# Performance work log

Measured on AMD Instinct MI355X. Metric: run time of the kernel, lower is better.

## Reference

```python
import jax, jax.numpy as jnp
import numpy as np

TAU = 2.0      # LIF time constant
VTH = 1.0      # spike threshold
ALPHA = 4.0    # sigmoid surrogate slope (spikingjelly default)
EPS = 1e-5     # BN eps

@jax.custom_vjp
def spike_fn(x):
    return (x >= 0.0).astype(x.dtype)

def _spike_fwd(x):
    return spike_fn(x), x

def _spike_bwd(x, g):
    s = jax.nn.sigmoid(ALPHA * x)
    return (g * ALPHA * s * (1.0 - s),)

spike_fn.defvjp(_spike_fwd, _spike_bwd)

def conv2d(x, w, stride=1):
    return jax.lax.conv_general_dilated(
        x, w, (stride, stride), 'SAME',
        dimension_numbers=('NCHW', 'OIHW', 'NCHW'))

def bn(x, g, b, m, v):
    # eval-mode BatchNorm2d over channel axis 1
    scale = g / jnp.sqrt(v + EPS)
    return (x - m[:, None, None]) * scale[:, None, None] + b[:, None, None]

def lif_step(v, x):
    # charge, fire, hard reset to 0 (detach_reset)
    v = v + (x - v) / TAU
    s = spike_fn(v - VTH)
    v = (1.0 - jax.lax.stop_gradient(s)) * v
    return v, s

def lif_multistep(x_seq):
    v0 = jnp.zeros_like(x_seq[0])
    _, s = jax.lax.scan(lif_step, v0, x_seq)
    return s

def setup_inputs():
    key = jax.random.key(0)
    ks = jax.random.split(key, 8)
    T, B, C, H, W = 4, 4, 2, 128, 128
    E = 256
    x = jax.random.normal(ks[0], (T, B, C, H, W), jnp.float32)
    w_proj = jax.random.normal(ks[1], (E // 2, C, 3, 3), jnp.float32) * 0.2
    w_temp = jax.random.normal(ks[2], (C, E // 2, 3, 3), jnp.float32) * 0.05
    w1 = jax.random.normal(ks[3], (E, E // 2, 3, 3), jnp.float32) * 0.03
    w_res = jax.random.normal(ks[4], (E, E // 2, 1, 1), jnp.float32) * 0.09
    def bn_params(k, c):
        kk = jax.random.split(k, 2)
        return (jnp.abs(jax.random.normal(kk[0], (c,), jnp.float32)) + 0.5,
                jax.random.normal(kk[1], (c,), jnp.float32) * 0.1,
                jnp.zeros((c,), jnp.float32), jnp.ones((c,), jnp.float32))
    g0, b0, m0, v0 = bn_params(ks[5], E // 2)
    gt, bt, mt, vt = bn_params(ks[6], C)
    g1, b1, m1, v1 = bn_params(ks[7], E)
    gr, br, mr, vr = bn_params(jax.random.fold_in(key, 99), E)
    return dict(x=x, w_proj=w_proj, g0=g0, b0=b0, m0=m0, v0=v0,
                w_temp=w_temp, gt=gt, bt=bt, mt=mt, vt=vt,
                w1=w1, g1=g1, b1=b1, m1=m1, v1=v1,
                w_res=w_res, gr=gr, br=br, mr=mr, vr=vr)

def reference(x, w_proj, g0, b0, m0, v0, w_temp, gt, bt, mt, vt,
              w1, g1, b1, m1, v1, w_res, gr, br, mr, vr):
    T, B, C, H, W = x.shape
    half = w_proj.shape[0]
    # stf_1 recurrent coding: x_in[t] = x[t] + x_out[t-1]; LIF states persist
    def step(carry, x_t):
        x_out, vp, vtm = carry
        x_in = x_t + x_out
        h = bn(conv2d(x_in, w_proj), g0, b0, m0, v0)          # [B,half,H,W]
        vp, s1 = lif_step(vp, h)                              # proj_lif
        y = bn(conv2d(s1, w_temp), gt, bt, mt, vt)            # [B,C,H,W]
        vtm, s2 = lif_step(vtm, y)                            # proj_temporal_lif
        return (s2, vp, vtm), s1
    init = (jnp.zeros((B, C, H, W), x.dtype),
            jnp.zeros((B, half, H, W), x.dtype),
            jnp.zeros((B, C, H, W), x.dtype))
    _, spikes = jax.lax.scan(step, init, x)                   # [T,B,half,H,W]
    xf = spikes.reshape(T * B, half, H, W)
    xa = bn(conv2d(xf, w1), g1, b1, m1, v1).reshape(T, B, -1, H, W)
    xa = lif_multistep(xa)                                    # proj1_lif
    xr = bn(conv2d(xf, w_res), gr, br, mr, vr).reshape(T, B, -1, H, W)
    xr = lif_multistep(xr)                                    # proj_res_lif
    return xa + xr
```

## Files before the change

### kernel.cpp

```cpp
#include <hip/hip_runtime.h>
#include <math.h>

#define HW 16384

typedef __attribute__((ext_vector_type(8))) _Float16 half8;
typedef __attribute__((ext_vector_type(4))) float f32x4;

__global__ __launch_bounds__(256)
void k_reorder2(const float* __restrict__ w1, const float* __restrict__ wres,
                const float* __restrict__ g1, const float* __restrict__ b1,
                const float* __restrict__ m1, const float* __restrict__ v1,
                const float* __restrict__ gr, const float* __restrict__ br,
                const float* __restrict__ mr, const float* __restrict__ vr,
                const float* __restrict__ g0, const float* __restrict__ v0,
                const float* __restrict__ gt, const float* __restrict__ vt,
                short* __restrict__ whi, short* __restrict__ wmid,
                short* __restrict__ rhi, short* __restrict__ rmid,
                float* __restrict__ bias1, float* __restrict__ biasr,
                float* __restrict__ psc, float* __restrict__ tsc) {
    int i = blockIdx.x * 256 + threadIdx.x;
    if (i < 294912) {
        int n = i / 1152, rem = i % 1152;
        int ic = rem / 9, tap = rem % 9;
        float sc = g1[n] / sqrtf(v1[n] + 1e-5f);
        float wv = (w1[i] * sc) * 4096.0f;
        _Float16 h = (_Float16)wv;
        float r1 = wv - (float)h;
        _Float16 m = (_Float16)r1;
        int kb = ic >> 5, q = (ic >> 3) & 3, j = ic & 7;
        size_t f = ((((size_t)(kb * 9 + tap)) * 4 + q) * 256 + n) * 8 + j;
        whi[f]  = __builtin_bit_cast(short, h);
        wmid[f] = __builtin_bit_cast(short, m);
    }
    if (i < 32768) {
        int n = i >> 7, ic = i & 127;
        float sc = gr[n] / sqrtf(vr[n] + 1e-5f);
        float wv = (wres[i] * sc) * 4096.0f;
        _Float16 h = (_Float16)wv;
        float r1 = wv - (float)h;
        _Float16 m = (_Float16)r1;
        int kb = ic >> 5, q = (ic >> 3) & 3, j = ic & 7;
        size_t f = (((size_t)kb * 4 + q) * 256 + n) * 8 + j;
        rhi[f]  = __builtin_bit_cast(short, h);
        rmid[f] = __builtin_bit_cast(short, m);
    }
    if (i < 256) {
        float sc1 = g1[i] / sqrtf(v1[i] + 1e-5f);
        bias1[i] = (b1[i] - m1[i] * sc1) * 4096.0f;
        float scr_ = gr[i] / sqrtf(vr[i] + 1e-5f);
        biasr[i] = (br[i] - mr[i] * scr_) * 4096.0f;
    }
    if (i < 128) psc[i] = g0[i] / sqrtf(v0[i] + 1e-5f);
    if (i < 2)   tsc[i] = gt[i] / sqrtf(vt[i] + 1e-5f);
}

__global__ __launch_bounds__(256)
void k_proj(const float* __restrict__ xt, const float* __restrict__ xout,
            const float* __restrict__ wp,
            const float* __restrict__ psc, const float* __restrict__ bb,
            const float* __restrict__ mm,
            float* __restrict__ vp, unsigned char* __restrict__ s1t,
            int first, int last) {
    __shared__ float xin[2 * 10 * 36];
    const int tid = threadIdx.x;
    const int b   = blockIdx.z >> 2;
    const int ocq = blockIdx.z & 3;
    const int gy0 = blockIdx.y * 8, gx0 = blockIdx.x * 32;

    for (int i = tid; i < 680; i += 256) {
        int ch = i / 340, rem = i % 340;
        int r = rem / 34, c = rem % 34;
        int gy = gy0 - 1 + r, gx = gx0 - 1 + c;
        float val = 0.f;
        if (gy >= 0 && gy < 128 && gx >= 0 && gx < 128) {
            int idx = ((b * 2 + ch) << 14) + (gy << 7) + gx;
            val = xt[idx];
            if (!first) val += xout[idx];
        }
        xin[(ch * 10 + r) * 36 + c] = val;
    }
    __syncthreads();

    const int prow = tid >> 5, pcol = tid & 31;
    float xw[2][3][3];
#pragma unroll
    for (int ch = 0; ch < 2; ++ch)
#pragma unroll
        for (int ky = 0; ky < 3; ++ky)
#pragma unroll
            for (int kx = 0; kx < 3; ++kx)
                xw[ch][ky][kx] = xin[(ch * 10 + prow + ky) * 36 + pcol + kx];

    const int pix = ((gy0 + prow) << 7) + gx0 + pcol;
    const int oc_beg = ocq * 32;
    unsigned int pk = 0u;
#pragma unroll
    for (int oo = 0; oo < 32; ++oo) {
        const int oc = oc_beg + oo;
        float acc = 0.f;
#pragma unroll
        for (int ch = 0; ch < 2; ++ch)
#pragma unroll
            for (int ky = 0; ky < 3; ++ky)
#pragma unroll
                for (int kx = 0; kx < 3; ++kx)
                    acc = fmaf(wp[((oc * 2 + ch) * 3 + ky) * 3 + kx], xw[ch][ky][kx], acc);
        float sc = psc[oc];
        float h  = (acc - mm[oc]) * sc + bb[oc];
        int idx = ((b * 128 + oc) << 14) + pix;
        float v = first ? 0.f : vp[idx];
        v = v + (h - v) * 0.5f;
        bool s = (v >= 1.0f);
        if (!last) vp[idx] = s ? 0.f : v;
        pk |= (s ? 1u : 0u) << oo;
    }
    *(unsigned int*)(s1t + ((((size_t)b << 14) + pix) << 4) + ocq * 4) = pk;
}

__global__ __launch_bounds__(256)
void k_temp(const unsigned char* __restrict__ s1t, const float* __restrict__ wt,
            const float* __restrict__ tsc, const float* __restrict__ bb,
            const float* __restrict__ mm,
            float* __restrict__ vtm, float* __restrict__ xout,
            int first, int lastv) {
    __shared__ unsigned char sl[49152];
    __shared__ float wls[2304];
    __shared__ float red[256];
    const int tid = threadIdx.x;
    const int b   = blockIdx.y;
    const int y0  = blockIdx.x;

    for (int i = tid; i < 2304; i += 256) wls[i] = wt[i];

    for (int i = tid; i < 384; i += 256) {
        int r = i >> 7, px = i & 127;
        int gy = y0 - 1 + r;
        uint4 d = make_uint4(0u, 0u, 0u, 0u);
        if (gy >= 0 && gy < 128)
            d = *(const uint4*)(s1t + ((((size_t)b << 14) + (gy << 7) + px) << 4));
        unsigned int bs[4] = {d.x, d.y, d.z, d.w};
#pragma unroll
        for (int icb = 0; icb < 16; ++icb) {
            unsigned int v8 = (bs[icb >> 2] >> ((icb & 3) * 8)) & 0xFFu;
            unsigned int lo = (v8 & 1u) | ((v8 & 2u) << 7) | ((v8 & 4u) << 14) | ((v8 & 8u) << 21);
            unsigned int hi = ((v8 >> 4) & 1u) | ((v8 & 32u) << 3) | ((v8 & 64u) << 10) | ((v8 & 128u) << 17);
            *(uint2*)&sl[(((icb * 3) + r) * 128 + (px ^ (icb & 7))) * 8] = make_uint2(lo, hi);
        }
    }
    __syncthreads();

    const int x = tid & 127, hf = tid >> 7;
    float a0 = 0.f, a1 = 0.f;
#pragma unroll 1
    for (int ii = 0; ii < 8; ++ii) {
        const int icb = hf * 8 + ii;
        int sw = icb & 7;
        const float* w0 = &wls[icb * 72];
        const float* w1_ = &wls[1152 + icb * 72];
#pragma unroll
        for (int dy = 0; dy < 3; ++dy) {
#pragma unroll
            for (int dx = 0; dx < 3; ++dx) {
                int xx = x - 1 + dx;
                if (xx < 0 || xx > 127) continue;
                uint2 d = *(const uint2*)&sl[((icb * 3 + dy) * 128 + (xx ^ sw)) * 8];
                int tap = dy * 3 + dx;
#pragma unroll
                for (int j = 0; j < 4; ++j) {
                    float f0 = (float)((d.x >> (8 * j)) & 0xFFu);
                    float f1 = (float)((d.y >> (8 * j)) & 0xFFu);
                    a0 = fmaf(w0[j * 9 + tap],        f0, a0);
                    a0 = fmaf(w0[(4 + j) * 9 + tap],  f1, a0);
                    a1 = fmaf(w1_[j * 9 + tap],       f0, a1);
                    a1 = fmaf(w1_[(4 + j) * 9 + tap], f1, a1);
                }
            }
        }
    }
    if (hf) { red[x] = a0; red[128 + x] = a1; }
    __syncthreads();
    if (!hf) {
        a0 += red[x]; a1 += red[128 + x];
#pragma unroll
        for (int oc = 0; oc < 2; ++oc) {
            float acc = (oc == 0) ? a0 : a1;
            float sc = tsc[oc];
            float yv = (acc - mm[oc]) * sc + bb[oc];
            int idx = ((b * 2 + oc) << 14) + (y0 << 7) + x;
            float v = first ? 0.f : vtm[idx];
            v = v + (yv - v) * 0.5f;
            bool s = (v >= 1.0f);
            if (!lastv) vtm[idx] = s ? 0.f : v;
            xout[idx] = s ? 1.0f : 0.f;
        }
    }
}

__global__ __launch_bounds__(256, 3)
void k_fused(const unsigned char* __restrict__ s1c,
             const short* __restrict__ whi, const short* __restrict__ wmid,
             const short* __restrict__ rhi, const short* __restrict__ rmid,
             const float* __restrict__ bias1, const float* __restrict__ biasr,
             float* __restrict__ out) {
    __shared__ __align__(16) unsigned char bl[8704];
    __shared__ __align__(16) unsigned char xp[34816];

    const int tid = threadIdx.x;
    const int oc0 = blockIdx.x * 64;
    const int yb = blockIdx.y;
    const int b = yb >> 8, ry = (yb >> 2) & 63, cx = yb & 3;
    const int gy0 = ry * 2, gx0 = cx * 32;

    const int w   = tid >> 6, l = tid & 63;
    const int q   = l >> 4,  ln = l & 15;
    const int woc = w >> 1,  wpx = w & 1;

    const size_t wofs = ((size_t)q * 256 + oc0 + woc * 32 + ln) * 8;

    int pb[2], po[2], eb[2];
#pragma unroll
    for (int nt = 0; nt < 2; ++nt) {
        int px = wpx * 32 + nt * 16 + ln;
        int prow = px >> 5, pcol = px & 31;
        pb[nt] = prow * 34 + pcol;
        po[nt] = ((gy0 + prow) << 7) + gx0 + pcol;
        eb[nt] = pb[nt] * 64 + q * 16;
    }

    for (int cc = tid; cc < 544; cc += 256) {
        int t = cc / 136, p = cc - t * 136;
        int r = p / 34, c = p - r * 34;
        int gy = gy0 - 1 + r, gx = gx0 - 1 + c;
        uint4 d = make_uint4(0u, 0u, 0u, 0u);
        if (gy >= 0 && gy < 128 && gx >= 0 && gx < 128)
            d = *(const uint4*)(s1c + (size_t)t * 1048576 +
                                ((((size_t)b << 14) + (gy << 7) + gx) << 4));
        *(uint4*)(bl + cc * 16) = d;
    }
    __syncthreads();

    const float ds_ = 0.000244140625f;

    unsigned int srb[4];
    {
        f32x4 brr[2];
#pragma unroll
        for (int mt = 0; mt < 2; ++mt)
#pragma unroll
            for (int rg = 0; rg < 4; ++rg)
                brr[mt][rg] = biasr[oc0 + woc * 32 + mt * 16 + q * 4 + rg];

        float vres[2][2][4];
#pragma unroll
        for (int nt = 0; nt < 2; ++nt)
#pragma unroll
            for (int mt = 0; mt < 2; ++mt)
#pragma unroll
                for (int rg = 0; rg < 4; ++rg) vres[nt][mt][rg] = 0.f;

#pragma unroll
        for (int t = 0; t < 4; ++t) {
            const unsigned char* blt = bl + t * 2176;
            f32x4 accr[2][2];
#pragma unroll
            for (int nt = 0; nt < 2; ++nt)
#pragma unroll
                for (int mt = 0; mt < 2; ++mt) accr[nt][mt] = brr[mt];

#pragma unroll
            for (int kb = 0; kb < 4; ++kb) {
                half8 B4[2];
#pragma unroll
                for (int nt = 0; nt < 2; ++nt) {
                    unsigned int v8 = blt[(pb[nt] + 35) * 16 + kb * 4 + q];
                    uint4 pk;
                    pk.x = ((v8 & 1u)          | ((v8 & 2u)   << 15)) * 0x3C00u;
                    pk.y = (((v8 >> 2) & 1u)   | ((v8 & 8u)   << 13)) * 0x3C00u;
                    pk.z = (((v8 >> 4) & 1u)   | ((v8 & 32u)  << 11)) * 0x3C00u;
                    pk.w = (((v8 >> 6) & 1u)   | ((v8 & 128u) << 9 )) * 0x3C00u;
                    B4[nt] = __builtin_bit_cast(half8, pk);
                }
                half8 RH[2], RM[2];
#pragma unroll
                for (int mt = 0; mt < 2; ++mt) {
                    RH[mt] = *(const half8*)(rhi  + wofs + (size_t)kb * 8192 + mt * 128);
                    RM[mt] = *(const half8*)(rmid + wofs + (size_t)kb * 8192 + mt * 128);
                }
#pragma unroll
                for (int nt = 0; nt < 2; ++nt)
#pragma unroll
                    for (int mt = 0; mt < 2; ++mt) {
                        accr[nt][mt] = __builtin_amdgcn_mfma_f32_16x16x32_f16(RH[mt], B4[nt], accr[nt][mt], 0, 0, 0);
                        accr[nt][mt] = __builtin_amdgcn_mfma_f32_16x16x32_f16(RM[mt], B4[nt], accr[nt][mt], 0, 0, 0);
                    }
            }

            unsigned int sb = 0u;
#pragma unroll
            for (int nt = 0; nt < 2; ++nt)
#pragma unroll
                for (int mt = 0; mt < 2; ++mt)
#pragma unroll
                    for (int rg = 0; rg < 4; ++rg) {
                        float hr = accr[nt][mt][rg] * ds_;
                        float u = vres[nt][mt][rg];
                        u = u + (hr - u) * 0.5f;
                        bool sr_ = (u >= 1.0f);
                        vres[nt][mt][rg] = sr_ ? 0.f : u;
                        sb |= (sr_ ? 1u : 0u) << (mt * 8 + rg * 2 + nt);
                    }
            srb[t] = sb;
        }
    }

    f32x4 acc[4][2][2];
#pragma unroll
    for (int mt = 0; mt < 2; ++mt)
#pragma unroll
        for (int rg = 0; rg < 4; ++rg) {
            float bv = bias1[oc0 + woc * 32 + mt * 16 + q * 4 + rg];
#pragma unroll
            for (int t = 0; t < 4; ++t)
#pragma unroll
                for (int nt = 0; nt < 2; ++nt) acc[t][nt][mt][rg] = bv;
        }

    const short* bh = whi  + wofs;
    const short* bm = wmid + wofs;
#pragma unroll 1
    for (int kb = 0; kb < 4; ++kb) {
        if (kb) __syncthreads();
        for (int cc = tid; cc < 2176; cc += 256) {
            int r = cc >> 2, c = cc & 3;
            unsigned int dw = *(const unsigned int*)(bl + r * 16 + kb * 4);
            unsigned int x0 = dw >> (c * 8);
            uint4 o;
            o.x = ((x0 & 1u)          | ((x0 & 2u)   << 15)) * 0x3C00u;
            o.y = (((x0 >> 2) & 1u)   | ((x0 & 8u)   << 13)) * 0x3C00u;
            o.z = (((x0 >> 4) & 1u)   | ((x0 & 32u)  << 11)) * 0x3C00u;
            o.w = (((x0 >> 6) & 1u)   | ((x0 & 128u) << 9 )) * 0x3C00u;
            *(uint4*)(xp + cc * 16) = o;
        }
        __syncthreads();

#pragma unroll
        for (int tap = 0; tap < 9; ++tap) {
            const int toff = ((tap / 3) * 34 + (tap % 3)) * 64;
            half8 AH[2], AM[2];
#pragma unroll
            for (int mt = 0; mt < 2; ++mt) {
                AH[mt] = *(const half8*)(bh + mt * 128);
                AM[mt] = *(const half8*)(bm + mt * 128);
            }
#pragma unroll
            for (int t = 0; t < 4; ++t) {
                half8 B4[2];
#pragma unroll
                for (int nt = 0; nt < 2; ++nt)
                    B4[nt] = *(const half8*)(xp + t * 8704 + eb[nt] + toff);
#pragma unroll
                for (int nt = 0; nt < 2; ++nt)
#pragma unroll
                    for (int mt = 0; mt < 2; ++mt) {
                        acc[t][nt][mt] = __builtin_amdgcn_mfma_f32_16x16x32_f16(AH[mt], B4[nt], acc[t][nt][mt], 0, 0, 0);
                        acc[t][nt][mt] = __builtin_amdgcn_mfma_f32_16x16x32_f16(AM[mt], B4[nt], acc[t][nt][mt], 0, 0, 0);
                    }
            }
            bh += 8192; bm += 8192;
        }
    }

    float va[2][2][4];
#pragma unroll
    for (int nt = 0; nt < 2; ++nt)
#pragma unroll
        for (int mt = 0; mt < 2; ++mt)
#pragma unroll
            for (int rg = 0; rg < 4; ++rg) va[nt][mt][rg] = 0.f;

#pragma unroll
    for (int t = 0; t < 4; ++t) {
        const size_t tb = ((size_t)((t * 4 + b) * 256 + oc0)) << 14;
#pragma unroll
        for (int mt = 0; mt < 2; ++mt)
#pragma unroll
            for (int rg = 0; rg < 4; ++rg) {
                const size_t ob = tb + ((size_t)(woc * 32 + mt * 16 + q * 4 + rg) << 14);
#pragma unroll
                for (int nt = 0; nt < 2; ++nt) {
                    float ha = acc[t][nt][mt][rg] * ds_;
                    float v = va[nt][mt][rg];
                    v = v + (ha - v) * 0.5f;
                    bool s = (v >= 1.0f);
                    va[nt][mt][rg] = s ? 0.f : v;
                    float sa = s ? 1.f : 0.f;
                    float sr = ((srb[t] >> (mt * 8 + rg * 2 + nt)) & 1u) ? 1.f : 0.f;
                    out[ob + po[nt]] = sa + sr;
                }
            }
    }
}

extern "C" void kernel_launch(void* const* d_in, const int* in_sizes, int n_in,
                              void* d_out, int out_size, void* d_ws, size_t ws_size,
                              hipStream_t stream) {
    const float* x      = (const float*)d_in[0];
    const float* w_proj = (const float*)d_in[1];
    const float* g0 = (const float*)d_in[2];
    const float* b0 = (const float*)d_in[3];
    const float* m0 = (const float*)d_in[4];
    const float* v0 = (const float*)d_in[5];
    const float* w_temp = (const float*)d_in[6];
    const float* gt = (const float*)d_in[7];
    const float* bt = (const float*)d_in[8];
    const float* mt = (const float*)d_in[9];
    const float* vt = (const float*)d_in[10];
    const float* w1 = (const float*)d_in[11];
    const float* g1 = (const float*)d_in[12];
    const float* b1 = (const float*)d_in[13];
    const float* m1 = (const float*)d_in[14];
    const float* v1 = (const float*)d_in[15];
    const float* w_res = (const float*)d_in[16];
    const float* gr = (const float*)d_in[17];
    const float* br = (const float*)d_in[18];
    const float* mr = (const float*)d_in[19];
    const float* vr = (const float*)d_in[20];

    char* ws = (char*)d_ws;
    unsigned char* s1c = (unsigned char*)ws;
    float* vp    = (float*)(ws + 4194304);
    float* vtm   = (float*)(ws + 37748736);
    float* xout  = (float*)(ws + 38273024);
    short* whi   = (short*)(ws + 38797312);
    short* wmid  = (short*)(ws + 39387136);
    short* rhi   = (short*)(ws + 39976960);
    short* rmid  = (short*)(ws + 40042496);
    float* bias1 = (float*)(ws + 40108032);
    float* biasr = (float*)(ws + 40109056);
    float* psc   = (float*)(ws + 40110080);
    float* tsc   = (float*)(ws + 40110592);

    k_reorder2<<<dim3(1152), dim3(256), 0, stream>>>(
        w1, w_res, g1, b1, m1, v1, gr, br, mr, vr, g0, v0, gt, vt,
        whi, wmid, rhi, rmid, bias1, biasr, psc, tsc);

    for (int t = 0; t < 4; ++t) {
        const float* xt = x + (size_t)t * 131072;
        unsigned char* s1t = s1c + (size_t)t * 1048576;
        k_proj<<<dim3(4, 16, 16), dim3(256), 0, stream>>>(
            xt, xout, w_proj, psc, b0, m0, vp, s1t, t == 0, t == 3);
        if (t < 3)
            k_temp<<<dim3(128, 4), dim3(256), 0, stream>>>(
                s1t, w_temp, tsc, bt, mt, vtm, xout, t == 0, t == 2);
    }

    k_fused<<<dim3(4, 1024), dim3(256), 0, stream>>>(
        s1c, whi, wmid, rhi, rmid, bias1, biasr, (float*)d_out);
}
```

Before: 618.0 us.

## Merge reorder, proj and temporal stages into one persistent kernel with grid barriers

Replaces the weight-reorder kernel and the seven per-timestep proj/temp launches with a single persistent kernel of 512 blocks. The blocks loop over tiles and separate the stages with a software grid barrier built on atomics. This removes the launch overhead and idle gaps between the small sequential kernels. In exchange it relies on all 512 blocks being co-resident (launch_bounds 256,2 with about 58KB of shared memory per block) to avoid deadlock, and it adds barrier spin cost.

Result: slower. 1.237 ms (+100.2%).

```diff
diff --git a/kernel.cpp b/kernel.cpp
--- a/kernel.cpp
+++ b/kernel.cpp
@@ -2,24 +2,55 @@
 #include <math.h>
 
 #define HW 16384
+#define NBLK 512
 
 typedef __attribute__((ext_vector_type(8))) _Float16 half8;
 typedef __attribute__((ext_vector_type(4))) float f32x4;
 
-__global__ __launch_bounds__(256)
-void k_reorder2(const float* __restrict__ w1, const float* __restrict__ wres,
-                const float* __restrict__ g1, const float* __restrict__ b1,
-                const float* __restrict__ m1, const float* __restrict__ v1,
-                const float* __restrict__ gr, const float* __restrict__ br,
-                const float* __restrict__ mr, const float* __restrict__ vr,
-                const float* __restrict__ g0, const float* __restrict__ v0,
-                const float* __restrict__ gt, const float* __restrict__ vt,
-                short* __restrict__ whi, short* __restrict__ wmid,
-                short* __restrict__ rhi, short* __restrict__ rmid,
-                float* __restrict__ bias1, float* __restrict__ biasr,
-                float* __restrict__ psc, float* __restrict__ tsc) {
-    int i = blockIdx.x * 256 + threadIdx.x;
-    if (i < 294912) {
+__device__ __forceinline__ void gsync(unsigned* bar, unsigned* lgen) {
+    __syncthreads();
+    if (threadIdx.x == 0) {
+        unsigned target = ++(*lgen);
+        __threadfence();
+        unsigned a = __hip_atomic_fetch_add(&bar[0], 1u, __ATOMIC_ACQ_REL,
+                                            __HIP_MEMORY_SCOPE_AGENT);
+        if (a == NBLK - 1) {
+            __hip_atomic_store(&bar[0], 0u, __ATOMIC_RELAXED, __HIP_MEMORY_SCOPE_AGENT);
+            __hip_atomic_fetch_add(&bar[1], 1u, __ATOMIC_RELEASE, __HIP_MEMORY_SCOPE_AGENT);
+        } else {
+            while (__hip_atomic_load(&bar[1], __ATOMIC_ACQUIRE,
+                                     __HIP_MEMORY_SCOPE_AGENT) < target)
+                __builtin_amdgcn_s_sleep(8);
+        }
+    }
+    __syncthreads();
+}
+
+__global__ __launch_bounds__(256, 2)
+void k_stage(const float* __restrict__ x, const float* __restrict__ wp,
+             const float* __restrict__ g0, const float* __restrict__ b0,
+             const float* __restrict__ m0, const float* __restrict__ v0,
+             const float* __restrict__ wt, const float* __restrict__ gt,
+             const float* __restrict__ bt, const float* __restrict__ mt,
+             const float* __restrict__ vt,
+             const float* __restrict__ w1, const float* __restrict__ g1,
+             const float* __restrict__ b1, const float* __restrict__ m1,
+             const float* __restrict__ v1,
+             const float* __restrict__ wres, const float* __restrict__ gr,
+             const float* __restrict__ br, const float* __restrict__ mr,
+             const float* __restrict__ vr,
+             unsigned char* __restrict__ s1c, float* __restrict__ vp,
+             float* __restrict__ vtm, float* xout,
+             short* __restrict__ whi, short* __restrict__ wmid,
+             short* __restrict__ rhi, short* __restrict__ rmid,
+             float* __restrict__ bias1, float* __restrict__ biasr,
+             float* __restrict__ psc, float* __restrict__ tsc,
+             unsigned* bar) {
+    __shared__ __align__(16) unsigned char smem[59392];
+    const int rb = blockIdx.x, tid = threadIdx.x;
+    unsigned lgen = 0;
+
+    for (int i = rb * 256 + tid; i < 294912; i += NBLK * 256) {
         int n = i / 1152, rem = i % 1152;
         int ic = rem / 9, tap = rem % 9;
         float sc = g1[n] / sqrtf(v1[n] + 1e-5f);
@@ -32,166 +63,169 @@
         whi[f]  = __builtin_bit_cast(short, h);
         wmid[f] = __builtin_bit_cast(short, m);
     }
-    if (i < 32768) {
-        int n = i >> 7, ic = i & 127;
-        float sc = gr[n] / sqrtf(vr[n] + 1e-5f);
-        float wv = (wres[i] * sc) * 4096.0f;
-        _Float16 h = (_Float16)wv;
-        float r1 = wv - (float)h;
-        _Float16 m = (_Float16)r1;
-        int kb = ic >> 5, q = (ic >> 3) & 3, j = ic & 7;
-        size_t f = (((size_t)kb * 4 + q) * 256 + n) * 8 + j;
-        rhi[f]  = __builtin_bit_cast(short, h);
-        rmid[f] = __builtin_bit_cast(short, m);
-    }
-    if (i < 256) {
-        float sc1 = g1[i] / sqrtf(v1[i] + 1e-5f);
-        bias1[i] = (b1[i] - m1[i] * sc1) * 4096.0f;
-        float scr_ = gr[i] / sqrtf(vr[i] + 1e-5f);
-        biasr[i] = (br[i] - mr[i] * scr_) * 4096.0f;
-    }
-    if (i < 128) psc[i] = g0[i] / sqrtf(v0[i] + 1e-5f);
-    if (i < 2)   tsc[i] = gt[i] / sqrtf(vt[i] + 1e-5f);
-}
-
-__global__ __launch_bounds__(256)
-void k_proj(const float* __restrict__ xt, const float* __restrict__ xout,
-            const float* __restrict__ wp,
-            const float* __restrict__ psc, const float* __restrict__ bb,
-            const float* __restrict__ mm,
-            float* __restrict__ vp, unsigned char* __restrict__ s1t,
-            int first, int last) {
-    __shared__ float xin[2 * 10 * 36];
-    const int tid = threadIdx.x;
-    const int b   = blockIdx.z >> 2;
-    const int ocq = blockIdx.z & 3;
-    const int gy0 = blockIdx.y * 8, gx0 = blockIdx.x * 32;
-
-    for (int i = tid; i < 680; i += 256) {
-        int ch = i / 340, rem = i % 340;
-        int r = rem / 34, c = rem % 34;
-        int gy = gy0 - 1 + r, gx = gx0 - 1 + c;
-        float val = 0.f;
-        if (gy >= 0 && gy < 128 && gx >= 0 && gx < 128) {
-            int idx = ((b * 2 + ch) << 14) + (gy << 7) + gx;
-            val = xt[idx];
-            if (!first) val += xout[idx];
-        }
-        xin[(ch * 10 + r) * 36 + c] = val;
-    }
-    __syncthreads();
-
-    const int prow = tid >> 5, pcol = tid & 31;
-    float xw[2][3][3];
-#pragma unroll
-    for (int ch = 0; ch < 2; ++ch)
-#pragma unroll
-        for (int ky = 0; ky < 3; ++ky)
-#pragma unroll
-            for (int kx = 0; kx < 3; ++kx)
-                xw[ch][ky][kx] = xin[(ch * 10 + prow + ky) * 36 + pcol + kx];
-
-    const int pix = ((gy0 + prow) << 7) + gx0 + pcol;
-    const int oc_beg = ocq * 32;
-    unsigned int pk = 0u;
-#pragma unroll
-    for (int oo = 0; oo < 32; ++oo) {
-        const int oc = oc_beg + oo;
-        float acc = 0.f;
-#pragma unroll
-        for (int ch = 0; ch < 2; ++ch)
-#pragma unroll
-            for (int ky = 0; ky < 3; ++ky)
-#pragma unroll
-                for (int kx = 0; kx < 3; ++kx)
-                    acc = fmaf(wp[((oc * 2 + ch) * 3 + ky) * 3 + kx], xw[ch][ky][kx], acc);
-        float sc = psc[oc];
-        float h  = (acc - mm[oc]) * sc + bb[oc];
-        int idx = ((b * 128 + oc) << 14) + pix;
-        float v = first ? 0.f : vp[idx];
-        v = v + (h - v) * 0.5f;
-        bool s = (v >= 1.0f);
-        if (!last) vp[idx] = s ? 0.f : v;
-        pk |= (s ? 1u : 0u) << oo;
-    }
-    *(unsigned int*)(s1t + ((((size_t)b << 14) + pix) << 4) + ocq * 4) = pk;
-}
-
-__global__ __launch_bounds__(256)
-void k_temp(const unsigned char* __restrict__ s1t, const float* __restrict__ wt,
-            const float* __restrict__ tsc, const float* __restrict__ bb,
-            const float* __restrict__ mm,
-            float* __restrict__ vtm, float* __restrict__ xout,
-            int first, int lastv) {
-    __shared__ unsigned char sl[49152];
-    __shared__ float wls[2304];
-    __shared__ float red[256];
-    const int tid = threadIdx.x;
-    const int b   = blockIdx.y;
-    const int y0  = blockIdx.x;
-
-    for (int i = tid; i < 2304; i += 256) wls[i] = wt[i];
-
-    for (int i = tid; i < 384; i += 256) {
-        int r = i >> 7, px = i & 127;
-        int gy = y0 - 1 + r;
-        uint4 d = make_uint4(0u, 0u, 0u, 0u);
-        if (gy >= 0 && gy < 128)
-            d = *(const uint4*)(s1t + ((((size_t)b << 14) + (gy << 7) + px) << 4));
-        unsigned int bs[4] = {d.x, d.y, d.z, d.w};
-#pragma unroll
-        for (int icb = 0; icb < 16; ++icb) {
-            unsigned int v8 = (bs[icb >> 2] >> ((icb & 3) * 8)) & 0xFFu;
-            unsigned int lo = (v8 & 1u) | ((v8 & 2u) << 7) | ((v8 & 4u) << 14) | ((v8 & 8u) << 21);
-            unsigned int hi = ((v8 >> 4) & 1u) | ((v8 & 32u) << 3) | ((v8 & 64u) << 10) | ((v8 & 128u) << 17);
-            *(uint2*)&sl[(((icb * 3) + r) * 128 + (px ^ (icb & 7))) * 8] = make_uint2(lo, hi);
-        }
-    }
-    __syncthreads();
-
-    const int x = tid & 127, hf = tid >> 7;
-    float a0 = 0.f, a1 = 0.f;
+    {
+        int i = rb * 256 + tid;
+        if (i < 32768) {
+            int n = i >> 7, ic = i & 127;
+            float sc = gr[n] / sqrtf(vr[n] + 1e-5f);
+            float wv = (wres[i] * sc) * 4096.0f;
+            _Float16 h = (_Float16)wv;
+            float r1 = wv - (float)h;
+            _Float16 m = (_Float16)r1;
+            int kb = ic >> 5, q = (ic >> 3) & 3, j = ic & 7;
+            size_t f = (((size_t)kb * 4 + q) * 256 + n) * 8 + j;
+            rhi[f]  = __builtin_bit_cast(short, h);
+            rmid[f] = __builtin_bit_cast(short, m);
+        }
+        if (i < 256) {
+            float sc1 = g1[i] / sqrtf(v1[i] + 1e-5f);
+            bias1[i] = (b1[i] - m1[i] * sc1) * 4096.0f;
+            float scr_ = gr[i] / sqrtf(vr[i] + 1e-5f);
+            biasr[i] = (br[i] - mr[i] * scr_) * 4096.0f;
+        }
+        if (i < 128) psc[i] = g0[i] / sqrtf(v0[i] + 1e-5f);
+        if (i < 2)   tsc[i] = gt[i] / sqrtf(vt[i] + 1e-5f);
+    }
+    gsync(bar, &lgen);
+
+    float* xin = (float*)smem;
+    unsigned char* sl = smem;
+    float* wls = (float*)(smem + 49152);
+    float* red = (float*)(smem + 49152 + 9216);
+
+    for (int t = 0; t < 4; ++t) {
+        const float* xt = x + (size_t)t * 131072;
+        unsigned char* s1t = s1c + (size_t)t * 1048576;
+        const int first = (t == 0), last = (t == 3);
+
+        for (int vtile = rb; vtile < 1024; vtile += NBLK) {
+            if (vtile != rb) __syncthreads();
+            const int bx = vtile & 3, by = (vtile >> 2) & 15, bz = vtile >> 6;
+            const int b   = bz >> 2;
+            const int ocq = bz & 3;
+            const int gy0 = by * 8, gx0 = bx * 32;
+
+            for (int i = tid; i < 680; i += 256) {
+                int ch = i / 340, rem = i % 340;
+                int r = rem / 34, c = rem % 34;
+                int gy = gy0 - 1 + r, gx = gx0 - 1 + c;
+                float val = 0.f;
+                if (gy >= 0 && gy < 128 && gx >= 0 && gx < 128) {
+                    int idx = ((b * 2 + ch) << 14) + (gy << 7) + gx;
+                    val = xt[idx];
+                    if (!first) val += xout[idx];
+                }
+                xin[(ch * 10 + r) * 36 + c] = val;
+            }
+            __syncthreads();
+
+            const int prow = tid >> 5, pcol = tid & 31;
+            float xw[2][3][3];
+#pragma unroll
+            for (int ch = 0; ch < 2; ++ch)
+#pragma unroll
+                for (int ky = 0; ky < 3; ++ky)
+#pragma unroll
+                    for (int kx = 0; kx < 3; ++kx)
+                        xw[ch][ky][kx] = xin[(ch * 10 + prow + ky) * 36 + pcol + kx];
+
+            const int pix = ((gy0 + prow) << 7) + gx0 + pcol;
+            const int oc_beg = ocq * 32;
+            unsigned int pk = 0u;
+#pragma unroll
+            for (int oo = 0; oo < 32; ++oo) {
+                const int oc = oc_beg + oo;
+                float acc = 0.f;
+#pragma unroll
+                for (int ch = 0; ch < 2; ++ch)
+#pragma unroll
+                    for (int ky = 0; ky < 3; ++ky)
+#pragma unroll
+                        for (int kx = 0; kx < 3; ++kx)
+                            acc = fmaf(wp[((oc * 2 + ch) * 3 + ky) * 3 + kx], xw[ch][ky][kx], acc);
+                float sc = psc[oc];
+                float h  = (acc - m0[oc]) * sc + b0[oc];
+                int idx = ((b * 128 + oc) << 14) + pix;
+                float v = first ? 0.f : vp[idx];
+                v = v + (h - v) * 0.5f;
+                bool s = (v >= 1.0f);
+                if (!last) vp[idx] = s ? 0.f : v;
+                pk |= (s ? 1u : 0u) << oo;
+            }
+            *(unsigned int*)(s1t + ((((size_t)b << 14) + pix) << 4) + ocq * 4) = pk;
+        }
+        gsync(bar, &lgen);
+
+        if (t < 3) {
+            const int lastv = (t == 2);
+            const int b  = rb >> 7;
+            const int y0 = rb & 127;
+
+            for (int i = tid; i < 2304; i += 256) wls[i] = wt[i];
+
+            for (int i = tid; i < 384; i += 256) {
+                int r = i >> 7, px = i & 127;
+                int gy = y0 - 1 + r;
+                uint4 d = make_uint4(0u, 0u, 0u, 0u);
+                if (gy >= 0 && gy < 128)
+                    d = *(const uint4*)(s1t + ((((size_t)b << 14) + (gy << 7) + px) << 4));
+                unsigned int bs[4] = {d.x, d.y, d.z, d.w};
+#pragma unroll
+                for (int icb = 0; icb < 16; ++icb) {
+                    unsigned int v8 = (bs[icb >> 2] >> ((icb & 3) * 8)) & 0xFFu;
+                    unsigned int lo = (v8 & 1u) | ((v8 & 2u) << 7) | ((v8 & 4u) << 14) | ((v8 & 8u) << 21);
+                    unsigned int hi = ((v8 >> 4) & 1u) | ((v8 & 32u) << 3) | ((v8 & 64u) << 10) | ((v8 & 128u) << 17);
+                    *(uint2*)&sl[(((icb * 3) + r) * 128 + (px ^ (icb & 7))) * 8] = make_uint2(lo, hi);
+                }
+            }
+            __syncthreads();
+
+            const int xx0 = tid & 127, hf = tid >> 7;
+            float a0 = 0.f, a1 = 0.f;
 #pragma unroll 1
-    for (int ii = 0; ii < 8; ++ii) {
-        const int icb = hf * 8 + ii;
-        int sw = icb & 7;
-        const float* w0 = &wls[icb * 72];
-        const float* w1_ = &wls[1152 + icb * 72];
-#pragma unroll
-        for (int dy = 0; dy < 3; ++dy) {
-#pragma unroll
-            for (int dx = 0; dx < 3; ++dx) {
-                int xx = x - 1 + dx;
-                if (xx < 0 || xx > 127) continue;
-                uint2 d = *(const uint2*)&sl[((icb * 3 + dy) * 128 + (xx ^ sw)) * 8];
-                int tap = dy * 3 + dx;
-#pragma unroll
-                for (int j = 0; j < 4; ++j) {
-                    float f0 = (float)((d.x >> (8 * j)) & 0xFFu);
-                    float f1 = (float)((d.y >> (8 * j)) & 0xFFu);
-                    a0 = fmaf(w0[j * 9 + tap],        f0, a0);
-                    a0 = fmaf(w0[(4 + j) * 9 + tap],  f1, a0);
-                    a1 = fmaf(w1_[j * 9 + tap],       f0, a1);
-                    a1 = fmaf(w1_[(4 + j) * 9 + tap], f1, a1);
-                }
-            }
-        }
-    }
-    if (hf) { red[x] = a0; red[128 + x] = a1; }
-    __syncthreads();
-    if (!hf) {
-        a0 += red[x]; a1 += red[128 + x];
-#pragma unroll
-        for (int oc = 0; oc < 2; ++oc) {
-            float acc = (oc == 0) ? a0 : a1;
-            float sc = tsc[oc];
-            float yv = (acc - mm[oc]) * sc + bb[oc];
-            int idx = ((b * 2 + oc) << 14) + (y0 << 7) + x;
-            float v = first ? 0.f : vtm[idx];
-            v = v + (yv - v) * 0.5f;
-            bool s = (v >= 1.0f);
-            if (!lastv) vtm[idx] = s ? 0.f : v;
-            xout[idx] = s ? 1.0f : 0.f;
+            for (int ii = 0; ii < 8; ++ii) {
+                const int icb = hf * 8 + ii;
+                int sw = icb & 7;
+                const float* w0 = &wls[icb * 72];
+                const float* w1_ = &wls[1152 + icb * 72];
+#pragma unroll
+                for (int dy = 0; dy < 3; ++dy) {
+#pragma unroll
+                    for (int dx = 0; dx < 3; ++dx) {
+                        int xx = xx0 - 1 + dx;
+                        if (xx < 0 || xx > 127) continue;
+                        uint2 d = *(const uint2*)&sl[((icb * 3 + dy) * 128 + (xx ^ sw)) * 8];
+                        int tap = dy * 3 + dx;
+#pragma unroll
+                        for (int j = 0; j < 4; ++j) {
+                            float f0 = (float)((d.x >> (8 * j)) & 0xFFu);
+                            float f1 = (float)((d.y >> (8 * j)) & 0xFFu);
+                            a0 = fmaf(w0[j * 9 + tap],        f0, a0);
+                            a0 = fmaf(w0[(4 + j) * 9 + tap],  f1, a0);
+                            a1 = fmaf(w1_[j * 9 + tap],       f0, a1);
+                            a1 = fmaf(w1_[(4 + j) * 9 + tap], f1, a1);
+                        }
+                    }
+                }
+            }
+            if (hf) { red[xx0] = a0; red[128 + xx0] = a1; }
+            __syncthreads();
+            if (!hf) {
+                a0 += red[xx0]; a1 += red[128 + xx0];
+#pragma unroll
+                for (int oc = 0; oc < 2; ++oc) {
+                    float acc = (oc == 0) ? a0 : a1;
+                    float sc = tsc[oc];
+                    float yv = (acc - mt[oc]) * sc + bt[oc];
+                    int idx = ((b * 2 + oc) << 14) + (y0 << 7) + xx0;
+                    float v = first ? 0.f : vtm[idx];
+                    v = v + (yv - v) * 0.5f;
+                    bool s = (v >= 1.0f);
+                    if (!lastv) vtm[idx] = s ? 0.f : v;
+                    xout[idx] = s ? 1.0f : 0.f;
+                }
+            }
+            gsync(bar, &lgen);
         }
     }
 }
@@ -245,18 +279,18 @@
     {
         f32x4 brr[2];
 #pragma unroll
-        for (int mt = 0; mt < 2; ++mt)
+        for (int mt2 = 0; mt2 < 2; ++mt2)
 #pragma unroll
             for (int rg = 0; rg < 4; ++rg)
-                brr[mt][rg] = biasr[oc0 + woc * 32 + mt * 16 + q * 4 + rg];
+                brr[mt2][rg] = biasr[oc0 + woc * 32 + mt2 * 16 + q * 4 + rg];
 
         float vres[2][2][4];
 #pragma unroll
         for (int nt = 0; nt < 2; ++nt)
 #pragma unroll
-            for (int mt = 0; mt < 2; ++mt)
-#pragma unroll
-                for (int rg = 0; rg < 4; ++rg) vres[nt][mt][rg] = 0.f;
+            for (int mt2 = 0; mt2 < 2; ++mt2)
+#pragma unroll
+                for (int rg = 0; rg < 4; ++rg) vres[nt][mt2][rg] = 0.f;
 
 #pragma unroll
         for (int t = 0; t < 4; ++t) {
@@ -265,7 +299,7 @@
 #pragma unroll
             for (int nt = 0; nt < 2; ++nt)
 #pragma unroll
-                for (int mt = 0; mt < 2; ++mt) accr[nt][mt] = brr[mt];
+                for (int mt2 = 0; mt2 < 2; ++mt2) accr[nt][mt2] = brr[mt2];
 
 #pragma unroll
             for (int kb = 0; kb < 4; ++kb) {
@@ -282,16 +316,16 @@
                 }
                 half8 RH[2], RM[2];
 #pragma unroll
-                for (int mt = 0; mt < 2; ++mt) {
-                    RH[mt] = *(const half8*)(rhi  + wofs + (size_t)kb * 8192 + mt * 128);
-                    RM[mt] = *(const half8*)(rmid + wofs + (size_t)kb * 8192 + mt * 128);
+                for (int mt2 = 0; mt2 < 2; ++mt2) {
+                    RH[mt2] = *(const half8*)(rhi  + wofs + (size_t)kb * 8192 + mt2 * 128);
+                    RM[mt2] = *(const half8*)(rmid + wofs + (size_t)kb * 8192 + mt2 * 128);
                 }
 #pragma unroll
                 for (int nt = 0; nt < 2; ++nt)
 #pragma unroll
-                    for (int mt = 0; mt < 2; ++mt) {
-                        accr[nt][mt] = __builtin_amdgcn_mfma_f32_16x16x32_f16(RH[mt], B4[nt], accr[nt][mt], 0, 0, 0);
-                        accr[nt][mt] = __builtin_amdgcn_mfma_f32_16x16x32_f16(RM[mt], B4[nt], accr[nt][mt], 0, 0, 0);
+                    for (int mt2 = 0; mt2 < 2; ++mt2) {
+                        accr[nt][mt2] = __builtin_amdgcn_mfma_f32_16x16x32_f16(RH[mt2], B4[nt], accr[nt][mt2], 0, 0, 0);
+                        accr[nt][mt2] = __builtin_amdgcn_mfma_f32_16x16x32_f16(RM[mt2], B4[nt], accr[nt][mt2], 0, 0, 0);
                     }
             }
 
@@ -299,15 +333,15 @@
 #pragma unroll
             for (int nt = 0; nt < 2; ++nt)
 #pragma unroll
-                for (int mt = 0; mt < 2; ++mt)
+                for (int mt2 = 0; mt2 < 2; ++mt2)
 #pragma unroll
                     for (int rg = 0; rg < 4; ++rg) {
-                        float hr = accr[nt][mt][rg] * ds_;
-                        float u = vres[nt][mt][rg];
+                        float hr = accr[nt][mt2][rg] * ds_;
+                        float u = vres[nt][mt2][rg];
                         u = u + (hr - u) * 0.5f;
                         bool sr_ = (u >= 1.0f);
-                        vres[nt][mt][rg] = sr_ ? 0.f : u;
-                        sb |= (sr_ ? 1u : 0u) << (mt * 8 + rg * 2 + nt);
+                        vres[nt][mt2][rg] = sr_ ? 0.f : u;
+                        sb |= (sr_ ? 1u : 0u) << (mt2 * 8 + rg * 2 + nt);
                     }
             srb[t] = sb;
         }
@@ -315,14 +349,14 @@
 
     f32x4 acc[4][2][2];
 #pragma unroll
-    for (int mt = 0; mt < 2; ++mt)
+    for (int mt2 = 0; mt2 < 2; ++mt2)
 #pragma unroll
         for (int rg = 0; rg < 4; ++rg) {
-            float bv = bias1[oc0 + woc * 32 + mt * 16 + q * 4 + rg];
+            float bv = bias1[oc0 + woc * 32 + mt2 * 16 + q * 4 + rg];
 #pragma unroll
             for (int t = 0; t < 4; ++t)
 #pragma unroll
-                for (int nt = 0; nt < 2; ++nt) acc[t][nt][mt][rg] = bv;
+                for (int nt = 0; nt < 2; ++nt) acc[t][nt][mt2][rg] = bv;
         }
 
     const short* bh = whi  + wofs;
@@ -348,9 +382,9 @@
             const int toff = ((tap / 3) * 34 + (tap % 3)) * 64;
             half8 AH[2], AM[2];
 #pragma unroll
-            for (int mt = 0; mt < 2; ++mt) {
-                AH[mt] = *(const half8*)(bh + mt * 128);
-                AM[mt] = *(const half8*)(bm + mt * 128);
+            for (int mt2 = 0; mt2 < 2; ++mt2) {
+                AH[mt2] = *(const half8*)(bh + mt2 * 128);
+                AM[mt2] = *(const half8*)(bm + mt2 * 128);
             }
 #pragma unroll
             for (int t = 0; t < 4; ++t) {
@@ -361,9 +395,9 @@
 #pragma unroll
                 for (int nt = 0; nt < 2; ++nt)
 #pragma unroll
-                    for (int mt = 0; mt < 2; ++mt) {
-                        acc[t][nt][mt] = __builtin_amdgcn_mfma_f32_16x16x32_f16(AH[mt], B4[nt], acc[t][nt][mt], 0, 0, 0);
-                        acc[t][nt][mt] = __builtin_amdgcn_mfma_f32_16x16x32_f16(AM[mt], B4[nt], acc[t][nt][mt], 0, 0, 0);
+                    for (int mt2 = 0; mt2 < 2; ++mt2) {
+                        acc[t][nt][mt2] = __builtin_amdgcn_mfma_f32_16x16x32_f16(AH[mt2], B4[nt], acc[t][nt][mt2], 0, 0, 0);
+                        acc[t][nt][mt2] = __builtin_amdgcn_mfma_f32_16x16x32_f16(AM[mt2], B4[nt], acc[t][nt][mt2], 0, 0, 0);
                     }
             }
             bh += 8192; bm += 8192;
@@ -374,27 +408,27 @@
 #pragma unroll
     for (int nt = 0; nt < 2; ++nt)
 #pragma unroll
-        for (int mt = 0; mt < 2; ++mt)
-#pragma unroll
-            for (int rg = 0; rg < 4; ++rg) va[nt][mt][rg] = 0.f;
+        for (int mt2 = 0; mt2 < 2; ++mt2)
+#pragma unroll
+            for (int rg = 0; rg < 4; ++rg) va[nt][mt2][rg] = 0.f;
 
 #pragma unroll
     for (int t = 0; t < 4; ++t) {
         const size_t tb = ((size_t)((t * 4 + b) * 256 + oc0)) << 14;
 #pragma unroll
-        for (int mt = 0; mt < 2; ++mt)
+        for (int mt2 = 0; mt2 < 2; ++mt2)
 #pragma unroll
             for (int rg = 0; rg < 4; ++rg) {
-                const size_t ob = tb + ((size_t)(woc * 32 + mt * 16 + q * 4 + rg) << 14);
+                const size_t ob = tb + ((size_t)(woc * 32 + mt2 * 16 + q * 4 + rg) << 14);
 #pragma unroll
                 for (int nt = 0; nt < 2; ++nt) {
-                    float ha = acc[t][nt][mt][rg] * ds_;
-                    float v = va[nt][mt][rg];
+                    float ha = acc[t][nt][mt2][rg] * ds_;
+                    float v = va[nt][mt2][rg];
                     v = v + (ha - v) * 0.5f;
                     bool s = (v >= 1.0f);
-                    va[nt][mt][rg] = s ? 0.f : v;
+                    va[nt][mt2][rg] = s ? 0.f : v;
                     float sa = s ? 1.f : 0.f;
-                    float sr = ((srb[t] >> (mt * 8 + rg * 2 + nt)) & 1u) ? 1.f : 0.f;
+                    float sr = ((srb[t] >> (mt2 * 8 + rg * 2 + nt)) & 1u) ? 1.f : 0.f;
                     out[ob + po[nt]] = sa + sr;
                 }
             }
@@ -439,20 +473,15 @@
     float* biasr = (float*)(ws + 40109056);
     float* psc   = (float*)(ws + 40110080);
     float* tsc   = (float*)(ws + 40110592);
-
-    k_reorder2<<<dim3(1152), dim3(256), 0, stream>>>(
-        w1, w_res, g1, b1, m1, v1, gr, br, mr, vr, g0, v0, gt, vt,
-        whi, wmid, rhi, rmid, bias1, biasr, psc, tsc);
-
-    for (int t = 0; t < 4; ++t) {
-        const float* xt = x + (size_t)t * 131072;
-        unsigned char* s1t = s1c + (size_t)t * 1048576;
-        k_proj<<<dim3(4, 16, 16), dim3(256), 0, stream>>>(
-            xt, xout, w_proj, psc, b0, m0, vp, s1t, t == 0, t == 3);
-        if (t < 3)
-            k_temp<<<dim3(128, 4), dim3(256), 0, stream>>>(
-                s1t, w_temp, tsc, bt, mt, vtm, xout, t == 0, t == 2);
-    }
+    unsigned* bar = (unsigned*)(ws + 40110600);
+
+    (void)hipMemsetAsync(bar, 0, 8, stream);
+
+    k_stage<<<dim3(NBLK), dim3(256), 0, stream>>>(
+        x, w_proj, g0, b0, m0, v0, w_temp, gt, bt, mt, vt,
+        w1, g1, b1, m1, v1, w_res, gr, br, mr, vr,
+        s1c, vp, vtm, xout, whi, wmid, rhi, rmid,
+        bias1, biasr, psc, tsc, bar);
 
     k_fused<<<dim3(4, 1024), dim3(256), 0, stream>>>(
         s1c, whi, wmid, rhi, rmid, bias1, biasr, (float*)d_out);
```
